# Kernel optimization log

Hardware: AMD Instinct MI355X
Metric: run time of the kernel (lower is better)

## Reference

```python
import jax, jax.numpy as jnp
import numpy as np

SIGMA = 20.0  # outlier threshold from FindOutliers


def setup_inputs() -> dict:
    key = jax.random.key(0)
    k1, k2, k3 = jax.random.split(key, 3)
    B, S, K, N = 4, 2048, 4096, 4096
    x = jax.random.normal(k1, (B, S, K), dtype=jnp.float32).astype(jnp.float16)
    # inject outlier columns (every 512th column scaled up) so |x| > sigma fires,
    # exercising the mixed sparse(outlier)/dense int8 decomposition
    x = (x.astype(jnp.float32).at[..., ::512].multiply(40.0)).astype(jnp.float16)
    weight = (jax.random.normal(k2, (N, K), dtype=jnp.float32) * 0.02).astype(jnp.float16)
    bias = (jax.random.normal(k3, (N,), dtype=jnp.float32) * 0.01).astype(jnp.float16)
    return {"x": x, "weight": weight, "bias": bias}


def reference(x, weight, bias):
    # x: [B, S, K] fp16; weight: [N, K] fp16; bias: [N] fp16
    B, S, K = x.shape
    N = weight.shape[0]
    xf = x.astype(jnp.float32).reshape(-1, K)            # [M, K]
    w32 = weight.astype(jnp.float32)                     # [N, K]

    # FindOutliers: columns of the flattened activation with any |value| > sigma
    out_mask = jnp.any(jnp.abs(xf) > SIGMA, axis=0)      # [K] bool

    # weight quantization: zero outlier columns, per-output-row symmetric int8 scale
    w_base = jnp.where(out_mask[None, :], 0.0, w32)      # [N, K]
    scale_col = (jnp.max(jnp.abs(w_base), axis=1) / 127.0).astype(jnp.float16).astype(jnp.float32)
    scale_col = jnp.maximum(scale_col, 1e-8)             # guard all-zero rows
    q_w = jnp.round(jnp.clip(w_base / scale_col[:, None], -128.0, 127.0)).astype(jnp.int8)

    # FindRowScaleF32: per-row symmetric int8 quantization of the activation
    scale_row = jnp.max(jnp.abs(xf), axis=1, keepdims=True) / 127.0   # [M, 1] fp32
    scale_row = jnp.maximum(scale_row, 1e-8)
    q_x = jnp.round(jnp.clip(xf / scale_row, -128.0, 127.0)).astype(jnp.int8)

    # int8 GEMM with int32 accumulation, fused dequant epilogue
    acc = jax.lax.dot_general(q_x, q_w, (((1,), (1,)), ((), ())),
                              preferred_element_type=jnp.int32)      # [M, N]
    y = acc.astype(jnp.float32) * scale_row * scale_col[None, :]

    # sparse outlier part in fp16-precision math: x[:, ind] @ weight[:, ind].T
    # (expressed as a masked dense GEMM for jit-static shapes; same math)
    y = y + (xf * out_mask[None, :]) @ (w32 * out_mask[None, :]).T

    y = y + bias.astype(jnp.float32)[None, :]
    return y.reshape(B, S, N).astype(jnp.float16)
```

## Files before the change

### kernel.cpp

```cpp
#include <hip/hip_runtime.h>
#include <hip/hip_fp16.h>
#include <stdint.h>

#define GAS __attribute__((address_space(1)))
#define LAS __attribute__((address_space(3)))

static constexpr int K_TOT = 4096;
static constexpr int N_TOT = 4096;
static constexpr int NO_CAP = 64;
static constexpr float SIGMA = 20.0f;

typedef int v4i __attribute__((ext_vector_type(4)));

__global__ __launch_bounds__(256) void k_init(int* __restrict__ mask) {
  mask[blockIdx.x * 256 + threadIdx.x] = 0;
}

__global__ __launch_bounds__(256) void k_quant_x(const float* __restrict__ x,
                                                 int8_t* __restrict__ qx,
                                                 float* __restrict__ scale_row,
                                                 int* __restrict__ mask) {
  const int lane = threadIdx.x & 63;
  const int wid  = threadIdx.x >> 6;
  const int m = blockIdx.x * 4 + wid;
  const float* xr = x + (size_t)m * K_TOT;

  float4 v[16];
  float amax = 0.0f;
#pragma unroll
  for (int it = 0; it < 16; ++it) {
    const int k0 = it * 256 + lane * 4;
    v[it] = *(const float4*)(xr + k0);
    const float a0 = fabsf(v[it].x), a1 = fabsf(v[it].y);
    const float a2 = fabsf(v[it].z), a3 = fabsf(v[it].w);
    amax = fmaxf(amax, fmaxf(fmaxf(a0, a1), fmaxf(a2, a3)));
    if (a0 > SIGMA) mask[k0 + 0] = 1;
    if (a1 > SIGMA) mask[k0 + 1] = 1;
    if (a2 > SIGMA) mask[k0 + 2] = 1;
    if (a3 > SIGMA) mask[k0 + 3] = 1;
  }
#pragma unroll
  for (int off = 32; off > 0; off >>= 1)
    amax = fmaxf(amax, __shfl_xor(amax, off));

  const float s = fmaxf(amax / 127.0f, 1e-8f);
  if (lane == 0) scale_row[m] = s;

  int8_t* qr = qx + (size_t)m * K_TOT;
#pragma unroll
  for (int it = 0; it < 16; ++it) {
    const int k0 = it * 256 + lane * 4;
    const int q0 = (int)rintf(fminf(fmaxf(v[it].x / s, -128.0f), 127.0f));
    const int q1 = (int)rintf(fminf(fmaxf(v[it].y / s, -128.0f), 127.0f));
    const int q2 = (int)rintf(fminf(fmaxf(v[it].z / s, -128.0f), 127.0f));
    const int q3 = (int)rintf(fminf(fmaxf(v[it].w / s, -128.0f), 127.0f));
    const uint32_t p = (uint32_t)(q0 & 0xFF) | ((uint32_t)(q1 & 0xFF) << 8) |
                       ((uint32_t)(q2 & 0xFF) << 16) | ((uint32_t)(q3 & 0xFF) << 24);
    *(uint32_t*)(qr + k0) = p;
  }
}

__global__ __launch_bounds__(256) void k_compact(const int* __restrict__ mask,
                                                 uint8_t* __restrict__ bitbytes,
                                                 int* __restrict__ ind,
                                                 int* __restrict__ count) {
  const int t = threadIdx.x;
  int local[16];
  int cnt = 0;
  uint32_t bits = 0;
#pragma unroll
  for (int j = 0; j < 16; ++j) {
    const int k = t * 16 + j;
    if (mask[k]) { bits |= (1u << j); local[cnt++] = k; }
  }
  bitbytes[2 * t]     = (uint8_t)(bits & 0xFF);
  bitbytes[2 * t + 1] = (uint8_t)((bits >> 8) & 0xFF);

  const int lane = t & 63, wid = t >> 6;
  int incl = cnt;
  for (int off = 1; off < 64; off <<= 1) {
    int o = __shfl_up(incl, off);
    if (lane >= off) incl += o;
  }
  __shared__ int wsum[4];
  if (lane == 63) wsum[wid] = incl;
  __syncthreads();
  int base = 0;
  for (int i = 0; i < wid; ++i) base += wsum[i];
  const int excl = base + incl - cnt;
  for (int j = 0; j < cnt; ++j) {
    const int pos = excl + j;
    if (pos < NO_CAP) ind[pos] = local[j];
  }
  if (t == 255) {
    const int tot = excl + cnt;
    *count = tot > NO_CAP ? NO_CAP : tot;
  }
}

__global__ __launch_bounds__(256) void k_quant_w(const float* __restrict__ w,
                                                 const uint8_t* __restrict__ bitbytes,
                                                 const int* __restrict__ ind,
                                                 const int* __restrict__ count,
                                                 int8_t* __restrict__ qw,
                                                 float* __restrict__ scale_col,
                                                 float* __restrict__ wo) {
  const int lane = threadIdx.x & 63;
  const int wid  = threadIdx.x >> 6;
  const int n = blockIdx.x * 4 + wid;
  const float* wr_ = w + (size_t)n * K_TOT;

  float4 v[16];
  float amax = 0.0f;
#pragma unroll
  for (int it = 0; it < 16; ++it) {
    const int k0 = it * 256 + lane * 4;
    v[it] = *(const float4*)(wr_ + k0);
    const uint32_t b = (uint32_t)(bitbytes[k0 >> 3] >> (k0 & 7));
    if (b & 1u) v[it].x = 0.0f;
    if (b & 2u) v[it].y = 0.0f;
    if (b & 4u) v[it].z = 0.0f;
    if (b & 8u) v[it].w = 0.0f;
    amax = fmaxf(amax, fmaxf(fmaxf(fabsf(v[it].x), fabsf(v[it].y)),
                             fmaxf(fabsf(v[it].z), fabsf(v[it].w))));
  }
#pragma unroll
  for (int off = 32; off > 0; off >>= 1)
    amax = fmaxf(amax, __shfl_xor(amax, off));

  float s = amax / 127.0f;
  s = __half2float(__float2half_rn(s));
  s = fmaxf(s, 1e-8f);
  if (lane == 0) scale_col[n] = s;

  int8_t* qr = qw + (size_t)n * K_TOT;
#pragma unroll
  for (int it = 0; it < 16; ++it) {
    const int k0 = it * 256 + lane * 4;
    const int q0 = (int)rintf(fminf(fmaxf(v[it].x / s, -128.0f), 127.0f));
    const int q1 = (int)rintf(fminf(fmaxf(v[it].y / s, -128.0f), 127.0f));
    const int q2 = (int)rintf(fminf(fmaxf(v[it].z / s, -128.0f), 127.0f));
    const int q3 = (int)rintf(fminf(fmaxf(v[it].w / s, -128.0f), 127.0f));
    const uint32_t p = (uint32_t)(q0 & 0xFF) | ((uint32_t)(q1 & 0xFF) << 8) |
                       ((uint32_t)(q2 & 0xFF) << 16) | ((uint32_t)(q3 & 0xFF) << 24);
    *(uint32_t*)(qr + k0) = p;
  }

  const int cnt = *count;
  if (lane < NO_CAP) {
    float val = 0.0f;
    if (lane < cnt) val = wr_[ind[lane]];
    wo[(size_t)n * NO_CAP + lane] = val;
  }
}

__global__ __launch_bounds__(256) void k_gather_xo(const float* __restrict__ x,
                                                   const int* __restrict__ ind,
                                                   const int* __restrict__ count,
                                                   float* __restrict__ xo) {
  const int m = blockIdx.x * 256 + threadIdx.x;
  const int cnt = *count;
  const int fill = cnt < 8 ? 8 : cnt;
  for (int j = 0; j < fill; ++j) {
    float val = 0.0f;
    if (j < cnt) val = x[(size_t)m * K_TOT + ind[j]];
    xo[(size_t)m * NO_CAP + j] = val;
  }
}

#define STAGE_A(h, kt, bufb) do { \
  __builtin_amdgcn_global_load_lds((const GAS void*)(qx + gAoff[0] + (size_t)(h)*128*K_TOT + (size_t)(kt)*128), \
      (LAS void*)(smem + (bufb)*32768 + (h)*16384 + ldsOff0), 16, 0, 0); \
  __builtin_amdgcn_global_load_lds((const GAS void*)(qx + gAoff[1] + (size_t)(h)*128*K_TOT + (size_t)(kt)*128), \
      (LAS void*)(smem + (bufb)*32768 + (h)*16384 + ldsOff1), 16, 0, 0); \
} while (0)

#define STAGE_B(h, kt, bufb) do { \
  __builtin_amdgcn_global_load_lds((const GAS void*)(qw + gBoff[0] + (size_t)(h)*128*K_TOT + (size_t)(kt)*128), \
      (LAS void*)(smem + 65536 + (bufb)*32768 + (h)*16384 + ldsOff0), 16, 0, 0); \
  __builtin_amdgcn_global_load_lds((const GAS void*)(qw + gBoff[1] + (size_t)(h)*128*K_TOT + (size_t)(kt)*128), \
      (LAS void*)(smem + 65536 + (bufb)*32768 + (h)*16384 + ldsOff1), 16, 0, 0); \
} while (0)

#define LDA(mq, bufb) do { \
  _Pragma("unroll") for (int i_ = 0; i_ < 4; ++i_) \
  _Pragma("unroll") for (int ks_ = 0; ks_ < 2; ++ks_) \
    a[i_][ks_] = *(const v4i*)(smem + aHalfBase + (bufb)*32768 + ((mq)*4 + i_)*2048 + ks_*1024 + rcSwz); \
} while (0)

#define LDB(dst, nq, bufb) do { \
  _Pragma("unroll") for (int i_ = 0; i_ < 2; ++i_) \
  _Pragma("unroll") for (int ks_ = 0; ks_ < 2; ++ks_) \
    dst[i_][ks_] = *(const v4i*)(smem + bHalfBase + (bufb)*32768 + (bColBlk + (nq)*2 + i_)*2048 + ks_*1024 + rcSwz); \
} while (0)

#define MM(mq, nq, bsrc) do { \
  _Pragma("unroll") for (int i_ = 0; i_ < 4; ++i_) \
  _Pragma("unroll") for (int j_ = 0; j_ < 2; ++j_) \
  _Pragma("unroll") for (int ks_ = 0; ks_ < 2; ++ks_) \
    acc[(mq)*4 + i_][(nq)*2 + j_] = __builtin_amdgcn_mfma_i32_16x16x64_i8( \
        a[i_][ks_], bsrc[j_][ks_], acc[(mq)*4 + i_][(nq)*2 + j_], 0, 0, 0); \
} while (0)

#define BAR() __builtin_amdgcn_s_barrier()
#define PHASE_MFMA(mq, nq, bsrc) do { \
  BAR(); \
  asm volatile("s_waitcnt lgkmcnt(0)" ::: "memory"); \
  __builtin_amdgcn_s_setprio(1); \
  MM(mq, nq, bsrc); \
  __builtin_amdgcn_s_setprio(0); \
  BAR(); \
} while (0)

__global__ __launch_bounds__(512, 2) void k_gemm8(const int8_t* __restrict__ qx,
                                                  const int8_t* __restrict__ qw,
                                                  const float* __restrict__ scale_row,
                                                  const float* __restrict__ scale_col,
                                                  const float* __restrict__ xo,
                                                  const float* __restrict__ wo,
                                                  const int* __restrict__ countp,
                                                  const float* __restrict__ bias,
                                                  float* __restrict__ out) {
  extern __shared__ int8_t smem[];
  constexpr int NT = K_TOT / 128;

  const int t = threadIdx.x;
  const int lane = t & 63;
  const int wid = t >> 6;
  const int wm = wid >> 2;
  const int wn = wid & 3;

  const int nbx = gridDim.x;
  const int nwg = gridDim.x * gridDim.y;
  int lin = blockIdx.y * nbx + blockIdx.x;
  lin = (lin & 7) * (nwg >> 3) + (lin >> 3);
  const int bm0 = (lin % nbx) * 256;
  const int bn0 = (lin / nbx) * 256;

  size_t gAoff[2], gBoff[2];
#pragma unroll
  for (int l = 0; l < 2; ++l) {
    const int f = l * 512 + t;
    const int rb = f >> 7, kb = (f >> 6) & 1, r = (f >> 2) & 15, c16 = f & 3;
    const int c16s = c16 ^ ((r & 8) ? 2 : 0);
    const int rowInHalf = rb * 16 + r;
    const int colByte = kb * 64 + c16s * 16;
    gAoff[l] = (size_t)(bm0 + rowInHalf) * K_TOT + colByte;
    gBoff[l] = (size_t)(bn0 + rowInHalf) * K_TOT + colByte;
  }
  const int ldsOff0 = wid * 1024;
  const int ldsOff1 = 8192 + wid * 1024;

  const int rr = lane & 15;
  const int rcSwz = rr * 64 + (((lane >> 4) * 16) ^ ((lane & 8) ? 32 : 0));
  const int aHalfBase = wm * 16384;
  const int bHalfBase = 65536 + (wn >> 1) * 16384;
  const int bColBlk = (wn & 1) * 4;

  v4i acc[8][4];
#pragma unroll
  for (int i = 0; i < 8; ++i)
#pragma unroll
    for (int j = 0; j < 4; ++j) acc[i][j] = (v4i){0, 0, 0, 0};
  v4i a[4][2], b0[2][2], b1[2][2];

  STAGE_B(0, 0, 0);
  STAGE_B(1, 0, 0);
  STAGE_A(0, 0, 0);
  STAGE_A(1, 0, 0);
  STAGE_B(0, 1, 1);
  STAGE_B(1, 1, 1);
  STAGE_A(0, 1, 1);
  asm volatile("s_waitcnt vmcnt(6)" ::: "memory");
  BAR();

#pragma unroll 2
  for (int t0 = 0; t0 < NT; ++t0) {
    const int buf = t0 & 1, nbuf = buf ^ 1;
    if (t0 + 1 < NT) STAGE_A(1, t0 + 1, nbuf);
    LDA(0, buf);
    LDB(b0, 0, buf);
    PHASE_MFMA(0, 0, b0);
    LDB(b1, 1, buf);
    PHASE_MFMA(0, 1, b1);
    if (t0 + 2 < NT) STAGE_B(0, t0 + 2, buf);
    LDA(1, buf);
    PHASE_MFMA(1, 1, b1);
    if (t0 + 2 < NT) {
      STAGE_B(1, t0 + 2, buf);
      STAGE_A(0, t0 + 2, buf);
    }
    if (t0 < NT - 2) {
      asm volatile("s_waitcnt vmcnt(6)" ::: "memory");
    } else {
      asm volatile("s_waitcnt vmcnt(0)" ::: "memory");
    }
    PHASE_MFMA(1, 0, b0);
  }

  const int cnt = *countp;
  const int col = lane & 15;
  const int row4 = (lane >> 4) * 4;

  float scn[4], bzn[4];
  int nn[4];
#pragma unroll
  for (int ni = 0; ni < 4; ++ni) {
    const int n = bn0 + wn * 64 + ni * 16 + col;
    nn[ni] = n;
    scn[ni] = scale_col[n];
    bzn[ni] = bias[n];
  }

  if (cnt <= 8) {
    float wv[4][8];
#pragma unroll
    for (int ni = 0; ni < 4; ++ni)
#pragma unroll
      for (int j = 0; j < 8; ++j) wv[ni][j] = wo[(size_t)nn[ni] * NO_CAP + j];
#pragma unroll
    for (int mi = 0; mi < 8; ++mi) {
#pragma unroll
      for (int r = 0; r < 4; ++r) {
        const int m = bm0 + wm * 128 + mi * 16 + row4 + r;
        const float srm = scale_row[m];
        float xv[8];
#pragma unroll
        for (int j = 0; j < 8; ++j) xv[j] = xo[(size_t)m * NO_CAP + j];
#pragma unroll
        for (int ni = 0; ni < 4; ++ni) {
          float y = (float)acc[mi][ni][r] * srm * scn[ni];
#pragma unroll
          for (int j = 0; j < 8; ++j) y += xv[j] * wv[ni][j];
          y += bzn[ni];
          out[(size_t)m * N_TOT + nn[ni]] = __half2float(__float2half_rn(y));
        }
      }
    }
  } else {
#pragma unroll
    for (int mi = 0; mi < 8; ++mi) {
#pragma unroll
      for (int r = 0; r < 4; ++r) {
        const int m = bm0 + wm * 128 + mi * 16 + row4 + r;
        const float srm = scale_row[m];
#pragma unroll
        for (int ni = 0; ni < 4; ++ni) {
          float y = (float)acc[mi][ni][r] * srm * scn[ni];
          for (int j = 0; j < cnt; ++j)
            y += xo[(size_t)m * NO_CAP + j] * wo[(size_t)nn[ni] * NO_CAP + j];
          y += bzn[ni];
          out[(size_t)m * N_TOT + nn[ni]] = __half2float(__float2half_rn(y));
        }
      }
    }
  }
}

extern "C" void kernel_launch(void* const* d_in, const int* in_sizes, int n_in,
                              void* d_out, int out_size, void* d_ws, size_t ws_size,
                              hipStream_t stream) {
  const float* x    = (const float*)d_in[0];
  const float* w    = (const float*)d_in[1];
  const float* bias = (const float*)d_in[2];
  float* out        = (float*)d_out;

  const int M = in_sizes[0] / K_TOT;

  char* ws = (char*)d_ws;
  const size_t OFF_SR   = 0;
  const size_t OFF_SC   = OFF_SR + sizeof(float) * (size_t)M;
  const size_t OFF_MASK = OFF_SC + sizeof(float) * (size_t)N_TOT;
  const size_t OFF_IND  = OFF_MASK + sizeof(int) * (size_t)K_TOT;
  const size_t OFF_CNT  = OFF_IND + sizeof(int) * (size_t)NO_CAP;
  const size_t OFF_BB   = OFF_CNT + 256;
  const size_t OFF_XO   = (OFF_BB + (size_t)(K_TOT / 8) + 255) & ~(size_t)255;
  const size_t OFF_WO   = OFF_XO + sizeof(float) * (size_t)M * NO_CAP;
  const size_t OFF_QX   = (OFF_WO + sizeof(float) * (size_t)N_TOT * NO_CAP + 255) & ~(size_t)255;
  const size_t OFF_QW   = OFF_QX + (size_t)M * K_TOT;

  float* scale_row  = (float*)(ws + OFF_SR);
  float* scale_col  = (float*)(ws + OFF_SC);
  int* mask         = (int*)(ws + OFF_MASK);
  int* ind          = (int*)(ws + OFF_IND);
  int* count        = (int*)(ws + OFF_CNT);
  uint8_t* bitbytes = (uint8_t*)(ws + OFF_BB);
  float* xo         = (float*)(ws + OFF_XO);
  float* wo         = (float*)(ws + OFF_WO);
  int8_t* qx        = (int8_t*)(ws + OFF_QX);
  int8_t* qw        = (int8_t*)(ws + OFF_QW);

  hipFuncSetAttribute((const void*)k_gemm8,
                      hipFuncAttributeMaxDynamicSharedMemorySize, 131072);

  hipLaunchKernelGGL(k_init, dim3(K_TOT / 256), dim3(256), 0, stream, mask);
  hipLaunchKernelGGL(k_quant_x, dim3(M / 4), dim3(256), 0, stream, x, qx, scale_row, mask);
  hipLaunchKernelGGL(k_compact, dim3(1), dim3(256), 0, stream, mask, bitbytes, ind, count);
  hipLaunchKernelGGL(k_quant_w, dim3(N_TOT / 4), dim3(256), 0, stream,
                     w, bitbytes, ind, count, qw, scale_col, wo);
  hipLaunchKernelGGL(k_gather_xo, dim3(M / 256), dim3(256), 0, stream, x, ind, count, xo);
  hipLaunchKernelGGL(k_gemm8, dim3(M / 256, N_TOT / 256), dim3(512), 131072, stream,
                     qx, qw, scale_row, scale_col, xo, wo, count, bias, out);
}
```

Before: 259.9 us.

## Triple-buffer A tiles in LDS and double-buffer B fragments in the int8 GEMM

Rewrites the int8 GEMM main loop. A tiles now rotate through three LDS buffers and B keeps two, so global-to-LDS prefetch runs further ahead, and the B register fragments alternate between two sets across an unrolled pair of k-tiles. Register fragment loads for the next phase are placed before the current phase's MFMAs. Global offsets move to 32-bit, which trims address arithmetic. The goal is to hide load latency behind MFMA work, at the cost of raising dynamic LDS from 128KB to 160KB and more registers per thread.

New measurement: 411.0 us. 58.1% more time.

```diff
diff --git a/kernel.cpp b/kernel.cpp
--- a/kernel.cpp
+++ b/kernel.cpp
@@ -168,48 +168,78 @@
   }
 }
 
-#define STAGE_A(h, kt, bufb) do { \
-  __builtin_amdgcn_global_load_lds((const GAS void*)(qx + gAoff[0] + (size_t)(h)*128*K_TOT + (size_t)(kt)*128), \
-      (LAS void*)(smem + (bufb)*32768 + (h)*16384 + ldsOff0), 16, 0, 0); \
-  __builtin_amdgcn_global_load_lds((const GAS void*)(qx + gAoff[1] + (size_t)(h)*128*K_TOT + (size_t)(kt)*128), \
-      (LAS void*)(smem + (bufb)*32768 + (h)*16384 + ldsOff1), 16, 0, 0); \
-} while (0)
-
-#define STAGE_B(h, kt, bufb) do { \
-  __builtin_amdgcn_global_load_lds((const GAS void*)(qw + gBoff[0] + (size_t)(h)*128*K_TOT + (size_t)(kt)*128), \
-      (LAS void*)(smem + 65536 + (bufb)*32768 + (h)*16384 + ldsOff0), 16, 0, 0); \
-  __builtin_amdgcn_global_load_lds((const GAS void*)(qw + gBoff[1] + (size_t)(h)*128*K_TOT + (size_t)(kt)*128), \
-      (LAS void*)(smem + 65536 + (bufb)*32768 + (h)*16384 + ldsOff1), 16, 0, 0); \
-} while (0)
-
-#define LDA(mq, bufb) do { \
+#define STAGE_A2(kt, AB) do { \
+  __builtin_amdgcn_global_load_lds((const GAS void*)(qx + gA0 + (size_t)(kt)*128), \
+      (LAS void*)(smem + (AB) + ldsOff0), 16, 0, 0); \
+  __builtin_amdgcn_global_load_lds((const GAS void*)(qx + gA1 + (size_t)(kt)*128), \
+      (LAS void*)(smem + (AB) + ldsOff1), 16, 0, 0); \
+  __builtin_amdgcn_global_load_lds((const GAS void*)(qx + gA0 + 128*(size_t)K_TOT + (size_t)(kt)*128), \
+      (LAS void*)(smem + (AB) + 16384 + ldsOff0), 16, 0, 0); \
+  __builtin_amdgcn_global_load_lds((const GAS void*)(qx + gA1 + 128*(size_t)K_TOT + (size_t)(kt)*128), \
+      (LAS void*)(smem + (AB) + 16384 + ldsOff1), 16, 0, 0); \
+} while (0)
+
+#define STAGE_B2(kt, BPAR) do { \
+  __builtin_amdgcn_global_load_lds((const GAS void*)(qw + gB0 + (size_t)(kt)*128), \
+      (LAS void*)(smem + 98304 + (BPAR)*32768 + ldsOff0), 16, 0, 0); \
+  __builtin_amdgcn_global_load_lds((const GAS void*)(qw + gB1 + (size_t)(kt)*128), \
+      (LAS void*)(smem + 98304 + (BPAR)*32768 + ldsOff1), 16, 0, 0); \
+  __builtin_amdgcn_global_load_lds((const GAS void*)(qw + gB0 + 128*(size_t)K_TOT + (size_t)(kt)*128), \
+      (LAS void*)(smem + 98304 + (BPAR)*32768 + 16384 + ldsOff0), 16, 0, 0); \
+  __builtin_amdgcn_global_load_lds((const GAS void*)(qw + gB1 + 128*(size_t)K_TOT + (size_t)(kt)*128), \
+      (LAS void*)(smem + 98304 + (BPAR)*32768 + 16384 + ldsOff1), 16, 0, 0); \
+} while (0)
+
+#define LDA_(dst, mq, ABOFF) do { \
   _Pragma("unroll") for (int i_ = 0; i_ < 4; ++i_) \
   _Pragma("unroll") for (int ks_ = 0; ks_ < 2; ++ks_) \
-    a[i_][ks_] = *(const v4i*)(smem + aHalfBase + (bufb)*32768 + ((mq)*4 + i_)*2048 + ks_*1024 + rcSwz); \
-} while (0)
-
-#define LDB(dst, nq, bufb) do { \
+    dst[i_][ks_] = *(const v4i*)(smem + (ABOFF) + aWave + ((mq)*4 + i_)*2048 + ks_*1024 + rcSwz); \
+} while (0)
+
+#define LDB_(dst, nq, BPAR) do { \
   _Pragma("unroll") for (int i_ = 0; i_ < 2; ++i_) \
   _Pragma("unroll") for (int ks_ = 0; ks_ < 2; ++ks_) \
-    dst[i_][ks_] = *(const v4i*)(smem + bHalfBase + (bufb)*32768 + (bColBlk + (nq)*2 + i_)*2048 + ks_*1024 + rcSwz); \
-} while (0)
-
-#define MM(mq, nq, bsrc) do { \
+    dst[i_][ks_] = *(const v4i*)(smem + 98304 + (BPAR)*32768 + bWave + (bColBlk + (nq)*2 + i_)*2048 + ks_*1024 + rcSwz); \
+} while (0)
+
+#define MM_(asrc, bsrc, MQ, NQ) do { \
   _Pragma("unroll") for (int i_ = 0; i_ < 4; ++i_) \
   _Pragma("unroll") for (int j_ = 0; j_ < 2; ++j_) \
   _Pragma("unroll") for (int ks_ = 0; ks_ < 2; ++ks_) \
-    acc[(mq)*4 + i_][(nq)*2 + j_] = __builtin_amdgcn_mfma_i32_16x16x64_i8( \
-        a[i_][ks_], bsrc[j_][ks_], acc[(mq)*4 + i_][(nq)*2 + j_], 0, 0, 0); \
-} while (0)
-
-#define BAR() __builtin_amdgcn_s_barrier()
-#define PHASE_MFMA(mq, nq, bsrc) do { \
-  BAR(); \
-  asm volatile("s_waitcnt lgkmcnt(0)" ::: "memory"); \
-  __builtin_amdgcn_s_setprio(1); \
-  MM(mq, nq, bsrc); \
-  __builtin_amdgcn_s_setprio(0); \
-  BAR(); \
+    acc[(MQ)*4 + i_][(NQ)*2 + j_] = __builtin_amdgcn_mfma_i32_16x16x64_i8( \
+        asrc[i_][ks_], bsrc[j_][ks_], acc[(MQ)*4 + i_][(NQ)*2 + j_], 0, 0, 0); \
+} while (0)
+
+#define BAR()  __builtin_amdgcn_s_barrier()
+#define PRIO1  __builtin_amdgcn_s_setprio(1)
+#define PRIO0  __builtin_amdgcn_s_setprio(0)
+#define VMC(n) asm volatile("s_waitcnt vmcnt(" #n ")" ::: "memory")
+
+#define TILE(T0, AC, AN, BPAR, B0C, B0N) do {                                 \
+                                    \
+  LDA_(a47, 1, AC);                                                           \
+  BAR();                                                                      \
+  PRIO1; MM_(a03, B0C, 0, 0); PRIO0;                                          \
+  BAR();                                                                      \
+                                        \
+  BAR();                                                                      \
+  PRIO1; MM_(a03, b1, 0, 1); PRIO0;                                           \
+  if ((T0) < NT - 2) { VMC(8); } else if ((T0) == NT - 2) { VMC(4); }         \
+  BAR();                                                                      \
+     \
+  LDA_(a03, 0, AN);                                                           \
+  if ((T0) + 2 < NT) { STAGE_B2((T0) + 2, BPAR); }                            \
+  BAR();                                                                      \
+  PRIO1; MM_(a47, b1, 1, 1); PRIO0;                                           \
+  if ((T0) < NT - 2) { VMC(8); } else if ((T0) == NT - 2) { VMC(0); }         \
+  BAR();                                                                      \
+                  \
+  LDB_(B0N, 0, (BPAR) ^ 1);                                                   \
+  LDB_(b1, 1, (BPAR) ^ 1);                                                    \
+  if ((T0) + 3 < NT) { STAGE_A2((T0) + 3, AC); }                              \
+  BAR();                                                                      \
+  PRIO1; MM_(a47, B0C, 1, 0); PRIO0;                                          \
+  BAR();                                                                      \
 } while (0)
 
 __global__ __launch_bounds__(512, 2) void k_gemm8(const int8_t* __restrict__ qx,
@@ -237,24 +267,25 @@
   const int bm0 = (lin % nbx) * 256;
   const int bn0 = (lin / nbx) * 256;
 
-  size_t gAoff[2], gBoff[2];
-#pragma unroll
-  for (int l = 0; l < 2; ++l) {
-    const int f = l * 512 + t;
-    const int rb = f >> 7, kb = (f >> 6) & 1, r = (f >> 2) & 15, c16 = f & 3;
-    const int c16s = c16 ^ ((r & 8) ? 2 : 0);
-    const int rowInHalf = rb * 16 + r;
-    const int colByte = kb * 64 + c16s * 16;
-    gAoff[l] = (size_t)(bm0 + rowInHalf) * K_TOT + colByte;
-    gBoff[l] = (size_t)(bn0 + rowInHalf) * K_TOT + colByte;
+  uint32_t gA0, gA1, gB0, gB1;
+  {
+    const int f0 = t, f1 = 512 + t;
+    const int rb0 = f0 >> 7, kb0 = (f0 >> 6) & 1, r0 = (f0 >> 2) & 15, c0 = f0 & 3;
+    const int rb1 = f1 >> 7, kb1 = (f1 >> 6) & 1, r1 = (f1 >> 2) & 15, c1 = f1 & 3;
+    const int c0s = c0 ^ ((r0 & 8) ? 2 : 0);
+    const int c1s = c1 ^ ((r1 & 8) ? 2 : 0);
+    gA0 = (uint32_t)((bm0 + rb0 * 16 + r0) * K_TOT + kb0 * 64 + c0s * 16);
+    gA1 = (uint32_t)((bm0 + rb1 * 16 + r1) * K_TOT + kb1 * 64 + c1s * 16);
+    gB0 = (uint32_t)((bn0 + rb0 * 16 + r0) * K_TOT + kb0 * 64 + c0s * 16);
+    gB1 = (uint32_t)((bn0 + rb1 * 16 + r1) * K_TOT + kb1 * 64 + c1s * 16);
   }
   const int ldsOff0 = wid * 1024;
   const int ldsOff1 = 8192 + wid * 1024;
 
   const int rr = lane & 15;
   const int rcSwz = rr * 64 + (((lane >> 4) * 16) ^ ((lane & 8) ? 32 : 0));
-  const int aHalfBase = wm * 16384;
-  const int bHalfBase = 65536 + (wn >> 1) * 16384;
+  const int aWave = wm * 16384;
+  const int bWave = (wn >> 1) * 16384;
   const int bColBlk = (wn & 1) * 4;
 
   v4i acc[8][4];
@@ -262,40 +293,26 @@
   for (int i = 0; i < 8; ++i)
 #pragma unroll
     for (int j = 0; j < 4; ++j) acc[i][j] = (v4i){0, 0, 0, 0};
-  v4i a[4][2], b0[2][2], b1[2][2];
-
-  STAGE_B(0, 0, 0);
-  STAGE_B(1, 0, 0);
-  STAGE_A(0, 0, 0);
-  STAGE_A(1, 0, 0);
-  STAGE_B(0, 1, 1);
-  STAGE_B(1, 1, 1);
-  STAGE_A(0, 1, 1);
-  asm volatile("s_waitcnt vmcnt(6)" ::: "memory");
+  v4i a03[4][2], a47[4][2], b0a[2][2], b0b[2][2], b1[2][2];
+
+  int ac = 0, an = 32768, aw = 65536;
+
+  STAGE_A2(0, 0);
+  STAGE_B2(0, 0);
+  STAGE_A2(1, 32768);
+  VMC(4);
   BAR();
-
-#pragma unroll 2
-  for (int t0 = 0; t0 < NT; ++t0) {
-    const int buf = t0 & 1, nbuf = buf ^ 1;
-    if (t0 + 1 < NT) STAGE_A(1, t0 + 1, nbuf);
-    LDA(0, buf);
-    LDB(b0, 0, buf);
-    PHASE_MFMA(0, 0, b0);
-    LDB(b1, 1, buf);
-    PHASE_MFMA(0, 1, b1);
-    if (t0 + 2 < NT) STAGE_B(0, t0 + 2, buf);
-    LDA(1, buf);
-    PHASE_MFMA(1, 1, b1);
-    if (t0 + 2 < NT) {
-      STAGE_B(1, t0 + 2, buf);
-      STAGE_A(0, t0 + 2, buf);
-    }
-    if (t0 < NT - 2) {
-      asm volatile("s_waitcnt vmcnt(6)" ::: "memory");
-    } else {
-      asm volatile("s_waitcnt vmcnt(0)" ::: "memory");
-    }
-    PHASE_MFMA(1, 0, b0);
+  LDA_(a03, 0, 0);
+  LDB_(b0a, 0, 0);
+  LDB_(b1, 1, 0);
+  STAGE_B2(1, 1);
+  STAGE_A2(2, 65536);
+
+  for (int t0 = 0; t0 < NT; t0 += 2) {
+    TILE(t0, ac, an, 0, b0a, b0b);
+    { int tmp = ac; ac = an; an = aw; aw = tmp; }
+    TILE(t0 + 1, ac, an, 1, b0b, b0a);
+    { int tmp = ac; ac = an; an = aw; aw = tmp; }
   }
 
   const int cnt = *countp;
@@ -391,7 +408,7 @@
   int8_t* qw        = (int8_t*)(ws + OFF_QW);
 
   hipFuncSetAttribute((const void*)k_gemm8,
-                      hipFuncAttributeMaxDynamicSharedMemorySize, 131072);
+                      hipFuncAttributeMaxDynamicSharedMemorySize, 163840);
 
   hipLaunchKernelGGL(k_init, dim3(K_TOT / 256), dim3(256), 0, stream, mask);
   hipLaunchKernelGGL(k_quant_x, dim3(M / 4), dim3(256), 0, stream, x, qx, scale_row, mask);
@@ -399,6 +416,6 @@
   hipLaunchKernelGGL(k_quant_w, dim3(N_TOT / 4), dim3(256), 0, stream,
                      w, bitbytes, ind, count, qw, scale_col, wo);
   hipLaunchKernelGGL(k_gather_xo, dim3(M / 256), dim3(256), 0, stream, x, ind, count, xo);
-  hipLaunchKernelGGL(k_gemm8, dim3(M / 256, N_TOT / 256), dim3(512), 131072, stream,
+  hipLaunchKernelGGL(k_gemm8, dim3(M / 256, N_TOT / 256), dim3(512), 163840, stream,
                      qx, qw, scale_row, scale_col, xo, wo, count, bias, out);
 }
```
